# Kernel optimization log

Measured on AMD Instinct MI355X. Metric: run time of the kernel, lower is better.

Reference implementation:

```python
import jax, jax.numpy as jnp
import numpy as np

N, E, IN, HID, H, C, NL, OUT = 50000, 500000, 384, 128, 8, 16, 3, 16
NEG_SLOPE = 0.2

def setup_inputs() -> dict:
    key = jax.random.key(0)
    ks = jax.random.split(key, 16)
    s = 0.1
    return {
        "x": jax.random.normal(ks[0], (N, IN), jnp.float32),
        "edge_index": jax.random.randint(ks[1], (2, E), 0, N, jnp.int32),
        "proj_w": jax.random.normal(ks[2], (IN, HID), jnp.float32) * s,
        "proj_b": jax.random.normal(ks[3], (HID,), jnp.float32) * s,
        "lin_w": jax.random.normal(ks[4], (NL, HID, HID), jnp.float32) * s,
        "att_src": jax.random.normal(ks[5], (NL, H, C), jnp.float32) * s,
        "att_dst": jax.random.normal(ks[6], (NL, H, C), jnp.float32) * s,
        "gat_b": jax.random.normal(ks[7], (NL, HID), jnp.float32) * s,
        "ln_g": jnp.ones((NL, HID), jnp.float32),
        "ln_b": jnp.zeros((NL, HID), jnp.float32),
        "cls_w1": jax.random.normal(ks[8], (HID, HID // 2), jnp.float32) * s,
        "cls_b1": jax.random.normal(ks[9], (HID // 2,), jnp.float32) * s,
        "cls_w2": jax.random.normal(ks[10], (HID // 2, OUT), jnp.float32) * s,
        "cls_b2": jax.random.normal(ks[11], (OUT,), jnp.float32) * s,
    }

def _layernorm(h, g, b, eps=1e-5):
    mu = jnp.mean(h, axis=-1, keepdims=True)
    var = jnp.var(h, axis=-1, keepdims=True)
    return (h - mu) * jax.lax.rsqrt(var + eps) * g + b

def _gat_layer(h, src, dst, w, a_src, a_dst, bias):
    # h: [N, HID]; per-head transform -> [N, H, C]
    xh = (h @ w).reshape(N, H, C)
    al_s = jnp.einsum('nhc,hc->nh', xh, a_src)   # [N, H]
    al_d = jnp.einsum('nhc,hc->nh', xh, a_dst)
    e = jax.nn.leaky_relu(al_s[src] + al_d[dst], NEG_SLOPE)  # [E+N, H]
    # segment softmax over incoming edges of each dst node
    m = jax.ops.segment_max(e, dst, num_segments=N)
    e = jnp.exp(e - m[dst])
    denom = jax.ops.segment_sum(e, dst, num_segments=N)
    alpha = e / (denom[dst] + 1e-16)
    msg = xh[src] * alpha[:, :, None]            # [E+N, H, C]
    out = jax.ops.segment_sum(msg, dst, num_segments=N)
    return out.reshape(N, H * C) + bias

def reference(x, edge_index, proj_w, proj_b, lin_w, att_src, att_dst, gat_b,
              ln_g, ln_b, cls_w1, cls_b1, cls_w2, cls_b2):
    loops = jnp.arange(N, dtype=edge_index.dtype)  # PyG GATConv adds self-loops
    src = jnp.concatenate([edge_index[0], loops])
    dst = jnp.concatenate([edge_index[1], loops])
    h = jax.nn.relu(x @ proj_w + proj_b)
    for l in range(NL):
        h_res = h
        h = _gat_layer(h, src, dst, lin_w[l], att_src[l], att_dst[l], gat_b[l])
        h = h + h_res
        h = jax.nn.relu(_layernorm(h, ln_g[l], ln_b[l]))
    logits = jax.nn.relu(h @ cls_w1 + cls_b1) @ cls_w2 + cls_b2
    return jax.nn.log_softmax(logits, axis=1)
```

## Files before the change

### kernel.cpp

```cpp
#include <hip/hip_runtime.h>
#include <hip/hip_bf16.h>
#include <math.h>

#define NN 50000
#define EE 500000
#define DIN 384
#define HIDD 128
#define NHEAD 8
#define OUTD 16

typedef __attribute__((ext_vector_type(8))) __bf16 bf16x8;
typedef __attribute__((ext_vector_type(4))) float f32x4;

__device__ __forceinline__ ushort f2bf(float f) {
  union { float f; unsigned u; } v; v.f = f;
  unsigned r = v.u + 0x7fffu + ((v.u >> 16) & 1u);
  return (ushort)(r >> 16);
}
__device__ __forceinline__ float bflo(unsigned w) {
  union { unsigned u; float f; } v; v.u = w << 16; return v.f;
}
__device__ __forceinline__ float bfhi(unsigned w) {
  union { unsigned u; float f; } v; v.u = w & 0xffff0000u; return v.f;
}

__global__ void zero_ints(int* p, int n) {
  int i = blockIdx.x * blockDim.x + threadIdx.x;
  if (i < n) p[i] = 0;
}

__global__ void hist_kernel(const int* __restrict__ dst, int* __restrict__ counts, int e) {
  int i = blockIdx.x * blockDim.x + threadIdx.x;
  if (i < e) atomicAdd(&counts[dst[i]], 1);
}

#define SCAN_BS 256
#define SCAN_NBLK ((NN + SCAN_BS - 1) / SCAN_BS)

__global__ __launch_bounds__(256) void partial_sums(const int* __restrict__ counts,
                                                    int* __restrict__ bsum, int n) {
  __shared__ int red[256];
  int i = blockIdx.x * 256 + threadIdx.x;
  red[threadIdx.x] = (i < n) ? counts[i] : 0;
  __syncthreads();
  #pragma unroll
  for (int off = 128; off; off >>= 1) {
    if (threadIdx.x < off) red[threadIdx.x] += red[threadIdx.x + off];
    __syncthreads();
  }
  if (threadIdx.x == 0) bsum[blockIdx.x] = red[0];
}

__global__ __launch_bounds__(256) void scan_bsums(const int* __restrict__ bsum,
                                                  int* __restrict__ boff, int nb) {
  __shared__ int buf[256];
  int t = threadIdx.x;
  int v = (t < nb) ? bsum[t] : 0;
  buf[t] = v;
  __syncthreads();
  #pragma unroll
  for (int off = 1; off < 256; off <<= 1) {
    int u = (t >= off) ? buf[t - off] : 0;
    __syncthreads();
    buf[t] += u;
    __syncthreads();
  }
  if (t < nb) boff[t] = buf[t] - v;
}

__global__ __launch_bounds__(256) void final_scan(const int* __restrict__ counts,
                                                  const int* __restrict__ boff,
                                                  int* __restrict__ rowptr,
                                                  int* __restrict__ woff, int n) {
  __shared__ int buf[256];
  int i = blockIdx.x * 256 + threadIdx.x;
  int t = threadIdx.x;
  int v = (i < n) ? counts[i] : 0;
  buf[t] = v;
  __syncthreads();
  #pragma unroll
  for (int off = 1; off < 256; off <<= 1) {
    int u = (t >= off) ? buf[t - off] : 0;
    __syncthreads();
    buf[t] += u;
    __syncthreads();
  }
  int excl = boff[blockIdx.x] + buf[t] - v;
  if (i < n) { rowptr[i] = excl; woff[i] = excl; }
  if (i == n - 1) rowptr[n] = excl + v;
}

__global__ void scatter_kernel(const int* __restrict__ src, const int* __restrict__ dst,
                               int* __restrict__ woff, int* __restrict__ col, int e) {
  int i = blockIdx.x * blockDim.x + threadIdx.x;
  if (i < e) {
    int p = atomicAdd(&woff[dst[i]], 1);
    col[p] = src[i];
  }
}

__global__ void prep_weights(const float* __restrict__ proj_w,
                             const float* __restrict__ lin_w,
                             const float* __restrict__ cls_w1,
                             const float* __restrict__ cls_w2,
                             ushort* __restrict__ wt) {
  int i = blockIdx.x * blockDim.x + threadIdx.x;
  if (i < 49152) {
    int k = i >> 7, n = i & 127;
    wt[n * 384 + k] = f2bf(proj_w[i]);
  } else if (i < 98304) {
    int j = i - 49152;
    int l = j >> 14, rem = j & 16383;
    int k = rem >> 7, n = rem & 127;
    wt[49152 + l * 16384 + n * 128 + k] = f2bf(lin_w[j]);
  } else if (i < 106496) {
    int j = i - 98304;
    int n = j >> 7, k = j & 127;
    wt[98304 + n * 128 + k] = f2bf(cls_w1[k * 64 + n]);
  } else if (i < 107520) {
    int j = i - 106496;
    int n = j >> 6, k = j & 63;
    wt[106496 + n * 64 + k] = f2bf(cls_w2[k * 16 + n]);
  }
}

#define LDS_STRIDE 72
template<typename AT, bool RELU_BIAS, bool ATT>
__global__ __launch_bounds__(256) void mfma_gemm64(const AT* __restrict__ A,
                                                   const ushort* __restrict__ Bt,
                                                   const float* __restrict__ bias,
                                                   ushort* __restrict__ C,
                                                   const float* __restrict__ att_s,
                                                   const float* __restrict__ att_d,
                                                   float* __restrict__ al_s,
                                                   float* __restrict__ al_d,
                                                   int M, int K) {
  __shared__ ushort sA[64 * LDS_STRIDE];
  __shared__ ushort sB[128 * LDS_STRIDE];
  const int tid = threadIdx.x;
  const int wave = tid >> 6, lane = tid & 63;
  const int q = lane >> 4, lm = lane & 15;
  const int wr = wave >> 1, wc = wave & 1;
  const int m0 = blockIdx.x * 64;

  f32x4 acc[2][4];
  #pragma unroll
  for (int i = 0; i < 2; i++)
    #pragma unroll
    for (int j = 0; j < 4; j++) acc[i][j] = {0.f, 0.f, 0.f, 0.f};

  for (int k0 = 0; k0 < K; k0 += 64) {
    __syncthreads();
    if constexpr (sizeof(AT) == 4) {
      #pragma unroll
      for (int p = 0; p < 4; ++p) {
        int idx = p * 256 + tid;
        int r = idx >> 4;
        int c = (idx & 15) << 2;
        int row = min(m0 + r, M - 1);
        float4 v = *(const float4*)((const float*)A + (size_t)row * K + k0 + c);
        ushort4 u;
        u.x = f2bf(v.x); u.y = f2bf(v.y); u.z = f2bf(v.z); u.w = f2bf(v.w);
        *(ushort4*)&sA[r * LDS_STRIDE + c] = u;
      }
    } else {
      #pragma unroll
      for (int p = 0; p < 2; ++p) {
        int idx = p * 256 + tid;
        int r = idx >> 3;
        int c = (idx & 7) << 3;
        int row = min(m0 + r, M - 1);
        *(bf16x8*)&sA[r * LDS_STRIDE + c] =
            *(const bf16x8*)((const ushort*)A + (size_t)row * K + k0 + c);
      }
    }
    #pragma unroll
    for (int p = 0; p < 4; ++p) {
      int idx = p * 256 + tid;
      int r = idx >> 3;
      int c = (idx & 7) << 3;
      *(bf16x8*)&sB[r * LDS_STRIDE + c] = *(const bf16x8*)(Bt + (size_t)r * K + k0 + c);
    }
    __syncthreads();
    #pragma unroll
    for (int ks = 0; ks < 2; ++ks) {
      bf16x8 af[2], bfv[4];
      #pragma unroll
      for (int t = 0; t < 2; ++t)
        af[t] = *(const bf16x8*)&sA[(wr * 32 + t * 16 + lm) * LDS_STRIDE + ks * 32 + q * 8];
      #pragma unroll
      for (int t = 0; t < 4; ++t)
        bfv[t] = *(const bf16x8*)&sB[(wc * 64 + t * 16 + lm) * LDS_STRIDE + ks * 32 + q * 8];
      #pragma unroll
      for (int i = 0; i < 2; ++i)
        #pragma unroll
        for (int j = 0; j < 4; ++j)
          acc[i][j] = __builtin_amdgcn_mfma_f32_16x16x32_bf16(af[i], bfv[j], acc[i][j], 0, 0, 0);
    }
  }
  float asw[4], adw[4];
  if constexpr (ATT) {
    #pragma unroll
    for (int j = 0; j < 4; ++j) {
      asw[j] = att_s[(wc * 4 + j) * 16 + lm];
      adw[j] = att_d[(wc * 4 + j) * 16 + lm];
    }
  }
  #pragma unroll
  for (int i = 0; i < 2; ++i) {
    #pragma unroll
    for (int r = 0; r < 4; ++r) {
      int row = m0 + wr * 32 + i * 16 + q * 4 + r;
      if (row < M) {
        #pragma unroll
        for (int j = 0; j < 4; ++j) {
          int colc = wc * 64 + j * 16 + lm;
          float v = acc[i][j][r];
          if (RELU_BIAS) { v += bias[colc]; v = fmaxf(v, 0.f); }
          C[(size_t)row * 128 + colc] = f2bf(v);
        }
      }
    }
  }
  if constexpr (ATT) {
    #pragma unroll
    for (int i = 0; i < 2; ++i) {
      #pragma unroll
      for (int j = 0; j < 4; ++j) {
        #pragma unroll
        for (int r = 0; r < 4; ++r) {
          float ss = acc[i][j][r] * asw[j];
          float dd = acc[i][j][r] * adw[j];
          #pragma unroll
          for (int off = 1; off < 16; off <<= 1) {
            ss += __shfl_xor(ss, off);
            dd += __shfl_xor(dd, off);
          }
          if (lm == 0) {
            int row = m0 + wr * 32 + i * 16 + q * 4 + r;
            if (row < M) {
              al_s[row * 8 + wc * 4 + j] = ss;
              al_d[row * 8 + wc * 4 + j] = dd;
            }
          }
        }
      }
    }
  }
}

__global__ __launch_bounds__(256) void gat_aggregate(
    const ushort* __restrict__ xh, const float* __restrict__ al_s,
    const float* __restrict__ al_d, const int* __restrict__ rowptr,
    const int* __restrict__ col, const ushort* __restrict__ h_res,
    const float* __restrict__ gb, const float* __restrict__ lng,
    const float* __restrict__ lnb, ushort* __restrict__ h_out, int n) {
  const int lane = threadIdx.x & 63;
  const int node = (blockIdx.x * blockDim.x + threadIdx.x) >> 6;
  if (node >= n) return;
  const int e8 = lane >> 3;
  const int hh = lane & 7;
  const int head = lane >> 3;
  const unsigned* xw_base = (const unsigned*)xh;

  const int start = rowptr[node], end = rowptr[node + 1];
  const int T = end - start + 1;
  const float ald_c = al_d[node * 8 + hh];

  float m = -INFINITY, denom = 0.f, acc0 = 0.f, acc1 = 0.f;

  for (int c = 0; c < T; c += 16) {
    int it0 = c + e8, it1 = c + 8 + e8;
    int idx0 = start + it0, idx1 = start + it1;
    int s0 = (it0 < T && idx0 < end) ? col[idx0] : node;
    int s1 = (it1 < T && idx1 < end) ? col[idx1] : node;

    unsigned xg0[8], xg1[8];
    #pragma unroll
    for (int j = 0; j < 8; ++j)
      if (c + j < T) {
        int sj = __shfl(s0, j * 8);
        xg0[j] = xw_base[(size_t)sj * 64 + lane];
      }
    #pragma unroll
    for (int j = 0; j < 8; ++j)
      if (c + 8 + j < T) {
        int sj = __shfl(s1, j * 8);
        xg1[j] = xw_base[(size_t)sj * 64 + lane];
      }

    float e0 = al_s[s0 * 8 + hh] + ald_c;
    e0 = (e0 > 0.f) ? e0 : 0.2f * e0;
    if (it0 >= T) e0 = -INFINITY;
    float e1 = al_s[s1 * 8 + hh] + ald_c;
    e1 = (e1 > 0.f) ? e1 : 0.2f * e1;
    if (it1 >= T) e1 = -INFINITY;

    float cm = fmaxf(e0, e1);
    cm = fmaxf(cm, __shfl_xor(cm, 8));
    cm = fmaxf(cm, __shfl_xor(cm, 16));
    cm = fmaxf(cm, __shfl_xor(cm, 32));
    float newm = fmaxf(m, __shfl(cm, head));
    float newm_c = __shfl(newm, hh * 8);
    float p0 = __expf(e0 - newm_c);
    float p1 = __expf(e1 - newm_c);
    float scale = __expf(m - newm);
    m = newm;

    denom *= scale; acc0 *= scale; acc1 *= scale;
    #pragma unroll
    for (int j = 0; j < 8; ++j)
      if (c + j < T) {
        float pj = __shfl(p0, j * 8 + head);
        denom += pj;
        acc0 = fmaf(pj, bflo(xg0[j]), acc0);
        acc1 = fmaf(pj, bfhi(xg0[j]), acc1);
      }
    #pragma unroll
    for (int j = 0; j < 8; ++j)
      if (c + 8 + j < T) {
        float pj = __shfl(p1, j * 8 + head);
        denom += pj;
        acc0 = fmaf(pj, bflo(xg1[j]), acc0);
        acc1 = fmaf(pj, bfhi(xg1[j]), acc1);
      }
  }

  float inv = 1.f / denom;
  int c0 = lane * 2, c1 = c0 + 1;
  unsigned ur = ((const unsigned*)h_res)[(size_t)node * 64 + lane];
  float v0 = acc0 * inv + gb[c0] + bflo(ur);
  float v1 = acc1 * inv + gb[c1] + bfhi(ur);
  float sum = v0 + v1;
  #pragma unroll
  for (int off = 32; off; off >>= 1) sum += __shfl_xor(sum, off);
  float mean = sum * (1.f / 128.f);
  float d0 = v0 - mean, d1 = v1 - mean;
  float sq = d0 * d0 + d1 * d1;
  #pragma unroll
  for (int off = 32; off; off >>= 1) sq += __shfl_xor(sq, off);
  float rstd = rsqrtf(sq * (1.f / 128.f) + 1e-5f);
  float o0 = fmaxf(d0 * rstd * lng[c0] + lnb[c0], 0.f);
  float o1 = fmaxf(d1 * rstd * lng[c1] + lnb[c1], 0.f);
  ((unsigned*)h_out)[(size_t)node * 64 + lane] =
      (unsigned)f2bf(o0) | ((unsigned)f2bf(o1) << 16);
}

#define CSTR 136
#define HSTR 72
__global__ __launch_bounds__(256) void classifier_mfma(
    const ushort* __restrict__ h, const ushort* __restrict__ w1t,
    const float* __restrict__ b1, const ushort* __restrict__ w2t,
    const float* __restrict__ b2, float* __restrict__ out, int n) {
  __shared__ ushort sA[128 * CSTR];
  __shared__ ushort sB[64 * CSTR];
  __shared__ ushort sHid[128 * HSTR];
  const int tid = threadIdx.x;
  const int wave = tid >> 6, lane = tid & 63;
  const int q = lane >> 4, lm = lane & 15;
  const int wr = wave >> 1, wc = wave & 1;
  const int m0 = blockIdx.x * 128;

  #pragma unroll
  for (int p = 0; p < 8; ++p) {
    int idx = p * 256 + tid;
    int r = idx >> 4;
    int c = (idx & 15) << 3;
    int row = min(m0 + r, n - 1);
    *(bf16x8*)&sA[r * CSTR + c] = *(const bf16x8*)(h + (size_t)row * 128 + c);
  }
  #pragma unroll
  for (int p = 0; p < 4; ++p) {
    int idx = p * 256 + tid;
    int r = idx >> 4;
    int c = (idx & 15) << 3;
    *(bf16x8*)&sB[r * CSTR + c] = *(const bf16x8*)(w1t + r * 128 + c);
  }
  __syncthreads();

  f32x4 acc[4][2];
  #pragma unroll
  for (int i = 0; i < 4; ++i)
    #pragma unroll
    for (int j = 0; j < 2; ++j) acc[i][j] = {0.f, 0.f, 0.f, 0.f};
  #pragma unroll
  for (int ks = 0; ks < 4; ++ks) {
    bf16x8 af[4], bfv[2];
    #pragma unroll
    for (int t = 0; t < 4; ++t)
      af[t] = *(const bf16x8*)&sA[(wr * 64 + t * 16 + lm) * CSTR + ks * 32 + q * 8];
    #pragma unroll
    for (int j = 0; j < 2; ++j)
      bfv[j] = *(const bf16x8*)&sB[(wc * 32 + j * 16 + lm) * CSTR + ks * 32 + q * 8];
    #pragma unroll
    for (int i = 0; i < 4; ++i)
      #pragma unroll
      for (int j = 0; j < 2; ++j)
        acc[i][j] = __builtin_amdgcn_mfma_f32_16x16x32_bf16(af[i], bfv[j], acc[i][j], 0, 0, 0);
  }
  #pragma unroll
  for (int i = 0; i < 4; ++i) {
    #pragma unroll
    for (int j = 0; j < 2; ++j) {
      int colc = wc * 32 + j * 16 + lm;
      float bb = b1[colc];
      #pragma unroll
      for (int r = 0; r < 4; ++r) {
        int row = wr * 64 + i * 16 + q * 4 + r;
        float v = fmaxf(acc[i][j][r] + bb, 0.f);
        sHid[row * HSTR + colc] = f2bf(v);
      }
    }
  }
  __syncthreads();

  f32x4 acc2[2] = {{0.f, 0.f, 0.f, 0.f}, {0.f, 0.f, 0.f, 0.f}};
  #pragma unroll
  for (int ks = 0; ks < 2; ++ks) {
    bf16x8 b2f = *(const bf16x8*)(w2t + lm * 64 + ks * 32 + q * 8);
    #pragma unroll
    for (int t = 0; t < 2; ++t) {
      bf16x8 a2 = *(const bf16x8*)&sHid[(wave * 32 + t * 16 + lm) * HSTR + ks * 32 + q * 8];
      acc2[t] = __builtin_amdgcn_mfma_f32_16x16x32_bf16(a2, b2f, acc2[t], 0, 0, 0);
    }
  }
  float bb2 = b2[lm];
  #pragma unroll
  for (int t = 0; t < 2; ++t) {
    #pragma unroll
    for (int r = 0; r < 4; ++r) {
      int row = m0 + wave * 32 + t * 16 + q * 4 + r;
      float lg = acc2[t][r] + bb2;
      float mx = lg;
      #pragma unroll
      for (int off = 8; off; off >>= 1) mx = fmaxf(mx, __shfl_xor(mx, off, 16));
      float se = __expf(lg - mx);
      #pragma unroll
      for (int off = 8; off; off >>= 1) se += __shfl_xor(se, off, 16);
      if (row < n) out[(size_t)row * 16 + lm] = lg - mx - __logf(se);
    }
  }
}

extern "C" void kernel_launch(void* const* d_in, const int* in_sizes, int n_in,
                              void* d_out, int out_size, void* d_ws, size_t ws_size,
                              hipStream_t stream) {
  const float* x       = (const float*)d_in[0];
  const int*   ei      = (const int*)d_in[1];
  const float* proj_w  = (const float*)d_in[2];
  const float* proj_b  = (const float*)d_in[3];
  const float* lin_w   = (const float*)d_in[4];
  const float* att_src = (const float*)d_in[5];
  const float* att_dst = (const float*)d_in[6];
  const float* gat_b   = (const float*)d_in[7];
  const float* ln_g    = (const float*)d_in[8];
  const float* ln_b    = (const float*)d_in[9];
  const float* cls_w1  = (const float*)d_in[10];
  const float* cls_b1  = (const float*)d_in[11];
  const float* cls_w2  = (const float*)d_in[12];
  const float* cls_b2  = (const float*)d_in[13];
  float* outp = (float*)d_out;

  const int N = NN, E = EE;
  ushort* wt   = (ushort*)d_ws;
  ushort* h0   = wt + 108544;
  ushort* h1   = h0 + (size_t)N * 128;
  ushort* xh_u = h1 + (size_t)N * 128;
  float* als   = (float*)(xh_u + (size_t)N * 128);
  float* ald   = als + (size_t)N * NHEAD;
  int* counts  = (int*)(ald + (size_t)N * NHEAD);
  int* rowptr  = counts + N;
  int* woff    = rowptr + N + 1;
  int* col     = woff + N;
  int* bsum    = col + E;
  int* boff    = bsum + SCAN_NBLK;

  const int* e_src = ei;
  const int* e_dst = ei + E;

  prep_weights<<<(107520 + 255) / 256, 256, 0, stream>>>(proj_w, lin_w, cls_w1, cls_w2, wt);

  zero_ints<<<(N + 255) / 256, 256, 0, stream>>>(counts, N);
  hist_kernel<<<(E + 255) / 256, 256, 0, stream>>>(e_dst, counts, E);
  partial_sums<<<SCAN_NBLK, 256, 0, stream>>>(counts, bsum, N);
  scan_bsums<<<1, 256, 0, stream>>>(bsum, boff, SCAN_NBLK);
  final_scan<<<SCAN_NBLK, 256, 0, stream>>>(counts, boff, rowptr, woff, N);
  scatter_kernel<<<(E + 255) / 256, 256, 0, stream>>>(e_src, e_dst, woff, col, E);

  const int gblocks = (N + 63) / 64;
  mfma_gemm64<float, true, false><<<gblocks, 256, 0, stream>>>(
      x, wt, proj_b, h0, nullptr, nullptr, nullptr, nullptr, N, DIN);

  ushort* hc = h0;
  ushort* hn = h1;
  for (int l = 0; l < 3; ++l) {
    mfma_gemm64<ushort, false, true><<<gblocks, 256, 0, stream>>>(
        hc, wt + 49152 + l * 16384, nullptr, xh_u,
        att_src + l * 128, att_dst + l * 128, als, ald, N, 128);
    gat_aggregate<<<(N + 3) / 4, 256, 0, stream>>>(
        xh_u, als, ald, rowptr, col, hc, gat_b + l * 128, ln_g + l * 128,
        ln_b + l * 128, hn, N);
    ushort* t = hc; hc = hn; hn = t;
  }
  classifier_mfma<<<(N + 127) / 128, 256, 0, stream>>>(
      hc, wt + 98304, cls_b1, wt + 106496, cls_b2, outp, N);
}
```

Measured before the change: 402.5 us.

## Double-buffer GEMM B tiles, load A directly to registers, shrink aggregate chunks

The MFMA GEMM now keeps K as a template constant, double-buffers the weight tile in LDS, and prefetches the next k-slice into registers while the current one computes. The A operand is loaded straight from global memory into MFMA fragment registers (converting fp32 to bf16 in registers), which removes the A LDS staging and one barrier per iteration. The GAT aggregation loop processes 8 edges per iteration instead of 16, computing softmax weights before issuing the feature gathers and dropping per-edge bounds checks. The trade-off is higher register pressure, less coalesced A loads, and fewer gathers in flight per aggregation iteration.

Result: no change. 398.9 us (-0.9%).

```diff
diff --git a/kernel.cpp b/kernel.cpp
--- a/kernel.cpp
+++ b/kernel.cpp
@@ -22,6 +22,12 @@
 }
 __device__ __forceinline__ float bfhi(unsigned w) {
   union { unsigned u; float f; } v; v.u = w & 0xffff0000u; return v.f;
+}
+__device__ __forceinline__ bf16x8 pack8(const float4& a, const float4& b) {
+  union { bf16x8 v; ushort u[8]; } r;
+  r.u[0] = f2bf(a.x); r.u[1] = f2bf(a.y); r.u[2] = f2bf(a.z); r.u[3] = f2bf(a.w);
+  r.u[4] = f2bf(b.x); r.u[5] = f2bf(b.y); r.u[6] = f2bf(b.z); r.u[7] = f2bf(b.w);
+  return r.v;
 }
 
 __global__ void zero_ints(int* p, int n) {
@@ -125,7 +131,7 @@
 }
 
 #define LDS_STRIDE 72
-template<typename AT, bool RELU_BIAS, bool ATT>
+template<typename AT, int KK, bool RELU_BIAS, bool ATT>
 __global__ __launch_bounds__(256) void mfma_gemm64(const AT* __restrict__ A,
                                                    const ushort* __restrict__ Bt,
                                                    const float* __restrict__ bias,
@@ -134,70 +140,114 @@
                                                    const float* __restrict__ att_d,
                                                    float* __restrict__ al_s,
                                                    float* __restrict__ al_d,
-                                                   int M, int K) {
-  __shared__ ushort sA[64 * LDS_STRIDE];
-  __shared__ ushort sB[128 * LDS_STRIDE];
+                                                   int M) {
+  constexpr int NIT = KK / 64;
+  constexpr bool F32A = (sizeof(AT) == 4);
+  __shared__ ushort sB[2][128 * LDS_STRIDE];
   const int tid = threadIdx.x;
   const int wave = tid >> 6, lane = tid & 63;
   const int q = lane >> 4, lm = lane & 15;
   const int wr = wave >> 1, wc = wave & 1;
   const int m0 = blockIdx.x * 64;
 
+  int br[4], bc[4];
+  #pragma unroll
+  for (int p = 0; p < 4; ++p) {
+    int idx = p * 256 + tid;
+    br[p] = idx >> 3;
+    bc[p] = (idx & 7) << 3;
+  }
+
+  const float* ap0f = nullptr; const float* ap1f = nullptr;
+  const ushort* ap0h = nullptr; const ushort* ap1h = nullptr;
+  {
+    int r0 = min(m0 + wr * 32 + lm, M - 1);
+    int r1 = min(m0 + wr * 32 + 16 + lm, M - 1);
+    if constexpr (F32A) {
+      ap0f = (const float*)A + (size_t)r0 * KK + q * 8;
+      ap1f = (const float*)A + (size_t)r1 * KK + q * 8;
+    } else {
+      ap0h = (const ushort*)A + (size_t)r0 * KK + q * 8;
+      ap1h = (const ushort*)A + (size_t)r1 * KK + q * 8;
+    }
+  }
+
   f32x4 acc[2][4];
   #pragma unroll
   for (int i = 0; i < 2; i++)
     #pragma unroll
     for (int j = 0; j < 4; j++) acc[i][j] = {0.f, 0.f, 0.f, 0.f};
 
-  for (int k0 = 0; k0 < K; k0 += 64) {
-    __syncthreads();
-    if constexpr (sizeof(AT) == 4) {
-      #pragma unroll
-      for (int p = 0; p < 4; ++p) {
-        int idx = p * 256 + tid;
-        int r = idx >> 4;
-        int c = (idx & 15) << 2;
-        int row = min(m0 + r, M - 1);
-        float4 v = *(const float4*)((const float*)A + (size_t)row * K + k0 + c);
-        ushort4 u;
-        u.x = f2bf(v.x); u.y = f2bf(v.y); u.z = f2bf(v.z); u.w = f2bf(v.w);
-        *(ushort4*)&sA[r * LDS_STRIDE + c] = u;
+  bf16x8 breg[2][4];
+  float4 af32[2][2][4];
+  bf16x8 abf[2][2][2];
+
+  auto loadB = [&](int buf, int k0) {
+    #pragma unroll
+    for (int p = 0; p < 4; ++p)
+      breg[buf][p] = *(const bf16x8*)(Bt + (size_t)br[p] * KK + k0 + bc[p]);
+  };
+  auto writeB = [&](int buf) {
+    #pragma unroll
+    for (int p = 0; p < 4; ++p)
+      *(bf16x8*)&sB[buf][br[p] * LDS_STRIDE + bc[p]] = breg[buf][p];
+  };
+  auto loadA = [&](int buf, int k0) {
+    if constexpr (F32A) {
+      #pragma unroll
+      for (int ks = 0; ks < 2; ++ks) {
+        af32[buf][0][ks * 2]     = *(const float4*)(ap0f + k0 + ks * 32);
+        af32[buf][0][ks * 2 + 1] = *(const float4*)(ap0f + k0 + ks * 32 + 4);
+        af32[buf][1][ks * 2]     = *(const float4*)(ap1f + k0 + ks * 32);
+        af32[buf][1][ks * 2 + 1] = *(const float4*)(ap1f + k0 + ks * 32 + 4);
       }
     } else {
       #pragma unroll
-      for (int p = 0; p < 2; ++p) {
-        int idx = p * 256 + tid;
-        int r = idx >> 3;
-        int c = (idx & 7) << 3;
-        int row = min(m0 + r, M - 1);
-        *(bf16x8*)&sA[r * LDS_STRIDE + c] =
-            *(const bf16x8*)((const ushort*)A + (size_t)row * K + k0 + c);
+      for (int ks = 0; ks < 2; ++ks) {
+        abf[buf][0][ks] = *(const bf16x8*)(ap0h + k0 + ks * 32);
+        abf[buf][1][ks] = *(const bf16x8*)(ap1h + k0 + ks * 32);
       }
     }
-    #pragma unroll
-    for (int p = 0; p < 4; ++p) {
-      int idx = p * 256 + tid;
-      int r = idx >> 3;
-      int c = (idx & 7) << 3;
-      *(bf16x8*)&sB[r * LDS_STRIDE + c] = *(const bf16x8*)(Bt + (size_t)r * K + k0 + c);
-    }
-    __syncthreads();
+  };
+  auto compute = [&](int buf) {
     #pragma unroll
     for (int ks = 0; ks < 2; ++ks) {
       bf16x8 af[2], bfv[4];
       #pragma unroll
-      for (int t = 0; t < 2; ++t)
-        af[t] = *(const bf16x8*)&sA[(wr * 32 + t * 16 + lm) * LDS_STRIDE + ks * 32 + q * 8];
+      for (int t = 0; t < 2; ++t) {
+        if constexpr (F32A)
+          af[t] = pack8(af32[buf][t][ks * 2], af32[buf][t][ks * 2 + 1]);
+        else
+          af[t] = abf[buf][t][ks];
+      }
       #pragma unroll
       for (int t = 0; t < 4; ++t)
-        bfv[t] = *(const bf16x8*)&sB[(wc * 64 + t * 16 + lm) * LDS_STRIDE + ks * 32 + q * 8];
+        bfv[t] = *(const bf16x8*)&sB[buf][(wc * 64 + t * 16 + lm) * LDS_STRIDE + ks * 32 + q * 8];
       #pragma unroll
       for (int i = 0; i < 2; ++i)
         #pragma unroll
         for (int j = 0; j < 4; ++j)
           acc[i][j] = __builtin_amdgcn_mfma_f32_16x16x32_bf16(af[i], bfv[j], acc[i][j], 0, 0, 0);
     }
-  }
+  };
+
+  loadB(0, 0);
+  loadA(0, 0);
+  writeB(0);
+  __syncthreads();
+  #pragma unroll
+  for (int it = 0; it < NIT; ++it) {
+    if (it + 1 < NIT) {
+      loadB((it + 1) & 1, (it + 1) * 64);
+      loadA((it + 1) & 1, (it + 1) * 64);
+    }
+    compute(it & 1);
+    if (it + 1 < NIT) {
+      writeB((it + 1) & 1);
+      __syncthreads();
+    }
+  }
+
   float asw[4], adw[4];
   if constexpr (ATT) {
     #pragma unroll
@@ -269,61 +319,37 @@
 
   float m = -INFINITY, denom = 0.f, acc0 = 0.f, acc1 = 0.f;
 
-  for (int c = 0; c < T; c += 16) {
-    int it0 = c + e8, it1 = c + 8 + e8;
-    int idx0 = start + it0, idx1 = start + it1;
-    int s0 = (it0 < T && idx0 < end) ? col[idx0] : node;
-    int s1 = (it1 < T && idx1 < end) ? col[idx1] : node;
-
-    unsigned xg0[8], xg1[8];
-    #pragma unroll
-    for (int j = 0; j < 8; ++j)
-      if (c + j < T) {
-        int sj = __shfl(s0, j * 8);
-        xg0[j] = xw_base[(size_t)sj * 64 + lane];
-      }
-    #pragma unroll
-    for (int j = 0; j < 8; ++j)
-      if (c + 8 + j < T) {
-        int sj = __shfl(s1, j * 8);
-        xg1[j] = xw_base[(size_t)sj * 64 + lane];
-      }
-
-    float e0 = al_s[s0 * 8 + hh] + ald_c;
-    e0 = (e0 > 0.f) ? e0 : 0.2f * e0;
-    if (it0 >= T) e0 = -INFINITY;
-    float e1 = al_s[s1 * 8 + hh] + ald_c;
-    e1 = (e1 > 0.f) ? e1 : 0.2f * e1;
-    if (it1 >= T) e1 = -INFINITY;
-
-    float cm = fmaxf(e0, e1);
+  for (int c = 0; c < T; c += 8) {
+    int it = c + e8;
+    bool valid = it < T;
+    int idx = start + it;
+    int s = (valid && idx < end) ? col[idx] : node;
+    float e = al_s[s * 8 + hh] + ald_c;
+    e = (e > 0.f) ? e : 0.2f * e;
+    if (!valid) e = -INFINITY;
+    float cm = e;
     cm = fmaxf(cm, __shfl_xor(cm, 8));
     cm = fmaxf(cm, __shfl_xor(cm, 16));
     cm = fmaxf(cm, __shfl_xor(cm, 32));
     float newm = fmaxf(m, __shfl(cm, head));
     float newm_c = __shfl(newm, hh * 8);
-    float p0 = __expf(e0 - newm_c);
-    float p1 = __expf(e1 - newm_c);
+    float p_lane = __expf(e - newm_c);
     float scale = __expf(m - newm);
     m = newm;
-
+    unsigned xg[8];
+    int sj[8];
+    #pragma unroll
+    for (int j = 0; j < 8; ++j) sj[j] = __shfl(s, j * 8);
+    #pragma unroll
+    for (int j = 0; j < 8; ++j) xg[j] = xw_base[(size_t)sj[j] * 64 + lane];
     denom *= scale; acc0 *= scale; acc1 *= scale;
     #pragma unroll
-    for (int j = 0; j < 8; ++j)
-      if (c + j < T) {
-        float pj = __shfl(p0, j * 8 + head);
-        denom += pj;
-        acc0 = fmaf(pj, bflo(xg0[j]), acc0);
-        acc1 = fmaf(pj, bfhi(xg0[j]), acc1);
-      }
-    #pragma unroll
-    for (int j = 0; j < 8; ++j)
-      if (c + 8 + j < T) {
-        float pj = __shfl(p1, j * 8 + head);
-        denom += pj;
-        acc0 = fmaf(pj, bflo(xg1[j]), acc0);
-        acc1 = fmaf(pj, bfhi(xg1[j]), acc1);
-      }
+    for (int j = 0; j < 8; ++j) {
+      float pj = __shfl(p_lane, j * 8 + head);
+      denom += pj;
+      acc0 = fmaf(pj, bflo(xg[j]), acc0);
+      acc1 = fmaf(pj, bfhi(xg[j]), acc1);
+    }
   }
 
   float inv = 1.f / denom;
@@ -488,15 +514,15 @@
   scatter_kernel<<<(E + 255) / 256, 256, 0, stream>>>(e_src, e_dst, woff, col, E);
 
   const int gblocks = (N + 63) / 64;
-  mfma_gemm64<float, true, false><<<gblocks, 256, 0, stream>>>(
-      x, wt, proj_b, h0, nullptr, nullptr, nullptr, nullptr, N, DIN);
+  mfma_gemm64<float, DIN, true, false><<<gblocks, 256, 0, stream>>>(
+      x, wt, proj_b, h0, nullptr, nullptr, nullptr, nullptr, N);
 
   ushort* hc = h0;
   ushort* hn = h1;
   for (int l = 0; l < 3; ++l) {
-    mfma_gemm64<ushort, false, true><<<gblocks, 256, 0, stream>>>(
+    mfma_gemm64<ushort, HIDD, false, true><<<gblocks, 256, 0, stream>>>(
         hc, wt + 49152 + l * 16384, nullptr, xh_u,
-        att_src + l * 128, att_dst + l * 128, als, ald, N, 128);
+        att_src + l * 128, att_dst + l * 128, als, ald, N);
     gat_aggregate<<<(N + 3) / 4, 256, 0, stream>>>(
         xh_u, als, ald, rowptr, col, hc, gat_b + l * 128, ln_g + l * 128,
         ln_b + l * 128, hn, N);
```
